# Performance work log

Measured on AMD Instinct MI355X. Metric: run time of the kernel, lower is better.

## Reference

```python
import jax, jax.numpy as jnp
import numpy as np

ACT_DIM, H, ZD, NZ, B, T, NS = 20, 64, 64, 5, 1024, 128, 1000


def setup_inputs() -> dict:
    key = jax.random.key(0)
    ks = jax.random.split(key, 24)
    w = lambda k, s: jax.random.normal(k, s, jnp.float32) * 0.1
    return {
        'acts': jax.random.randint(ks[0], (B, T), 0, ACT_DIM, dtype=jnp.int32),
        'durs': jax.random.uniform(ks[1], (B, T), jnp.float32),
        'W_act': w(ks[2], (ACT_DIM, H)), 'b_act': jnp.zeros(H, jnp.float32),
        'W_dur': w(ks[3], (1, H)), 'b_dur': jnp.zeros(H, jnp.float32),
        'W_x': w(ks[4], (2 * H, H)), 'b_x': jnp.zeros(H, jnp.float32),
        'W_z': w(ks[5], (ZD, H)), 'b_z': jnp.zeros(H, jnp.float32),
        'Wp1': w(ks[6], (NZ, 2 * H, H)), 'bp1': jnp.zeros((NZ, H), jnp.float32),
        'Wp2': w(ks[7], (NZ, H, ZD)), 'bp2': jnp.zeros((NZ, ZD), jnp.float32),
        'Wq1': w(ks[8], (NZ, H, ZD)), 'bq1': jnp.zeros((NZ, ZD), jnp.float32),
        'Wq2': w(ks[9], (NZ, ZD, ZD)), 'bq2': jnp.zeros((NZ, ZD), jnp.float32),
        'W_dec': w(ks[10], (2 * H, H)), 'b_dec': jnp.zeros(H, jnp.float32),
        'W_a': w(ks[11], (H, ACT_DIM)), 'b_a': jnp.zeros(ACT_DIM, jnp.float32),
        'W_durd': w(ks[12], (2 * H, 1)), 'b_durd': jnp.zeros(1, jnp.float32),
        'W_ih': w(ks[13], (2 * H, 3 * H)), 'W_hh': w(ks[14], (H, 3 * H)),
        'b_ih': jnp.zeros(3 * H, jnp.float32), 'b_hh': jnp.zeros(3 * H, jnp.float32),
        'gamma_post': jnp.ones((1, NZ), jnp.float32),
        'gamma_prior': jnp.ones((1, NZ), jnp.float32),
    }


def reference(acts, durs, W_act, b_act, W_dur, b_dur, W_x, b_x, W_z, b_z,
              Wp1, bp1, Wp2, bp2, Wq1, bq1, Wq2, bq2, W_dec, b_dec,
              W_a, b_a, W_durd, b_durd, W_ih, W_hh, b_ih, b_hh,
              gamma_post, gamma_prior):
    relu, sp = jax.nn.relu, jax.nn.softplus
    Bn, Tn = acts.shape
    hd = W_hh.shape[0]
    rngkey = jax.random.key(42)

    # Precompute per-timestep input embeddings, vectorized over T.
    one_hot = jax.nn.one_hot(acts, W_act.shape[0], dtype=jnp.float32)   # (B,T,A)
    phi_act = relu(one_hot @ W_act + b_act)                              # (B,T,H)
    phi_dur = relu(durs[..., None] * W_dur[0] + b_dur)                   # (B,T,H)
    phi_x_all = relu(jnp.concatenate([phi_act, phi_dur], -1) @ W_x + b_x)
    phi_x_all = jnp.swapaxes(phi_x_all, 0, 1)                            # (T,B,H)

    # NOTE: the torch code computes mu and sigma from the SAME network output
    # (identical pre-activation), so we compute it once. gamma matmul: (1,nz)@(B,nz,z)->(B,1,z)
    def mix_post(inp):
        h1 = relu(jnp.einsum('bi,nio->bno', inp, Wp1) + bp1)
        pre = jnp.einsum('bno,noz->bnz', h1, Wp2) + bp2
        m = jnp.einsum('on,bnz->boz', gamma_post, pre)
        return relu(m), sp(m)

    def mix_prior(h):
        h1 = relu(jnp.einsum('bi,nio->bno', h, Wq1) + bq1)
        pre = jnp.einsum('bno,noz->bnz', h1, Wq2) + bq2
        m = jnp.einsum('on,bnz->boz', gamma_prior, pre)
        return relu(m), sp(m)

    def gru(x, h):
        gi = x @ W_ih + b_ih
        gh = h @ W_hh + b_hh
        ir, iz, inn = jnp.split(gi, 3, -1)
        hr, hz, hn = jnp.split(gh, 3, -1)
        r = jax.nn.sigmoid(ir + hr)
        zz = jax.nn.sigmoid(iz + hz)
        n = jnp.tanh(inn + r * hn)
        return (1.0 - zz) * n + zz * h

    def sample_mean(k, mu, sigma):
        eps = jnp.mean(jax.random.normal(k, (NS,) + mu.shape, mu.dtype), 0)
        return (mu + sigma * eps)[:, 0, :]

    def kl(m1, s1, m2, s2):  # diag-normal KL, summed over z (Independent, 1)
        return jnp.sum(jnp.log(s2 / s1) + (s1 ** 2 + (m1 - m2) ** 2) / (2.0 * s2 ** 2) - 0.5, -1)

    def step(carry, xs):
        h, kld = carry
        phi_x, t = xs
        pm, ps = mix_post(jnp.concatenate([phi_x, h], -1))
        qm, qs = mix_prior(h)
        kld = kld + kl(pm, ps, qm, qs)
        z = sample_mean(jax.random.fold_in(rngkey, t), pm, ps)
        phi_z = relu(z @ W_z + b_z)
        h = gru(jnp.concatenate([phi_x, phi_z], -1), h)
        return (h, kld), None

    h0 = jnp.zeros((Bn, hd), jnp.float32)
    (h, kld), _ = jax.lax.scan(step, (h0, jnp.zeros((Bn, 1), jnp.float32)),
                               (phi_x_all, jnp.arange(Tn)))

    qm, qs = mix_prior(h)
    z = sample_mean(jax.random.fold_in(rngkey, Tn), qm, qs)
    phi_z = relu(z @ W_z + b_z)
    dec = relu(jnp.concatenate([phi_z, h], -1) @ W_dec + b_dec)
    logits = dec @ W_a + b_a
    phi_logits = relu(logits @ W_act + b_act)
    dur_dec = jnp.concatenate([phi_logits, dec], -1) @ W_durd + b_durd
    return logits, (dur_dec, sp(dur_dec)), jnp.mean(kld)
```

## Files before the change

### kernel.cpp

```cpp
#include <hip/hip_runtime.h>
#include <hip/hip_bf16.h>
#include <math.h>


#define TT   128
#define NZN  5
#define ADIM 20
#define ROWS 16
#define FRW  38
#define PS   68

typedef __attribute__((ext_vector_type(8))) short short8;
typedef __attribute__((ext_vector_type(4))) float f32x4;

__device__ __forceinline__ float reluf(float x) { return fmaxf(x, 0.f); }
__device__ __forceinline__ float frcp(float x)  { return __builtin_amdgcn_rcpf(x); }
__device__ __forceinline__ float fexp(float x)  { return __expf(x); }
__device__ __forceinline__ float flog(float x)  { return __logf(x); }
__device__ __forceinline__ float fsigm(float x) { return frcp(1.f + fexp(-x)); }
__device__ __forceinline__ float ftanh(float x) {
    float cx = fminf(fmaxf(x, -15.f), 15.f);
    float e2 = fexp(2.f * cx);
    return 1.f - 2.f * frcp(e2 + 1.f);
}
__device__ __forceinline__ float fsoftplus(float x) {
    return fmaxf(x, 0.f) + flog(1.f + fexp(-fabsf(x)));
}
__device__ __forceinline__ unsigned int pk2bf(float lo, float hi) {
    unsigned int r;
    asm volatile("v_cvt_pk_bf16_f32 %0, %1, %2" : "=v"(r) : "v"(lo), "v"(hi));
    return r;
}
__device__ __forceinline__ short8 pack8(float v0, float v1, float v2, float v3,
                                        float v4, float v5, float v6, float v7) {
    union { short8 s; unsigned int u[4]; } r;
    r.u[0] = pk2bf(v0, v1); r.u[1] = pk2bf(v2, v3);
    r.u[2] = pk2bf(v4, v5); r.u[3] = pk2bf(v6, v7);
    return r.s;
}
__device__ __forceinline__ void stage2(short* buf, int shift, int rw0, int col,
                                       float v0, float v1) {
    unsigned int u = pk2bf(v0, v1);
    buf[(rw0 << shift) + (col ^ ((rw0 & 7) << 3))]             = (short)(u & 0xffff);
    buf[((rw0 + 1) << shift) + (col ^ (((rw0 + 1) & 7) << 3))] = (short)(u >> 16);
}
__device__ __forceinline__ short8 lda64(const short* b, int c, int col0) {
    return *(const short8*)(b + c * 64 + (col0 ^ ((c & 7) << 3)));
}
__device__ __forceinline__ short8 lda128(const short* b, int c, int col0) {
    return *(const short8*)(b + c * 128 + (col0 ^ ((c & 7) << 3)));
}
__device__ __forceinline__ unsigned short f2bf(float x) {
    union { float f; unsigned int u; } v; v.f = x;
    unsigned int r = v.u + 0x7fffu + ((v.u >> 16) & 1u);
    return (unsigned short)(r >> 16);
}
__device__ __forceinline__ float wave_sum64(float v) {
#pragma unroll
    for (int off = 32; off > 0; off >>= 1) v += __shfl_xor(v, off, 64);
    return v;
}
#define MFMA(a, b, acc) __builtin_amdgcn_mfma_f32_16x16x32_bf16((a), (b), (acc), 0, 0, 0)

__global__ void vrnn_zero(float* out) { out[22528] = 0.f; }

__global__ __launch_bounds__(256) void vrnn_pack(
    const float* __restrict__ W_x,  const float* __restrict__ Wp1,
    const float* __restrict__ Wq1,  const float* __restrict__ Wp2,
    const float* __restrict__ Wq2,  const float* __restrict__ W_z,
    const float* __restrict__ W_ih, const float* __restrict__ W_hh,
    short* __restrict__ ws)
{
    const int tid = blockIdx.x * blockDim.x + threadIdx.x;
    if (tid >= 8 * FRW * 64) return;
    const int l = tid & 63, f = (tid >> 6) % FRW, w = (tid >> 6) / FRW;
    const int cc = l & 15, gg = l >> 4;
    const float* src = nullptr; int ld = 64, ncol = 0, k0 = 0;
    if (w < 4) {
        const int fcp = 16 * w + cc; ncol = fcp;
        if (f < 4)       { src = W_x;  k0 = 32 * f; }
        else if (f < 20) { int r = f - 4;  int n = r >> 2, q = r & 3;
                           src = Wp1 + n * 8192; k0 = 32 * q; }
        else if (f < 30) { int r = f - 20; int n = r >> 1, q = r & 1;
                           src = Wp2 + n * 4096; k0 = 32 * q; }
        else if (f < 32) { src = W_z;  k0 = 32 * (f - 30); }
        else             { int r = f - 32; int gt = r >> 1, q = r & 1;
                           src = W_ih; ld = 192; ncol = gt * 64 + fcp; k0 = 64 + 32 * q; }
    } else {
        const int fcp = 16 * (w - 4) + cc; ncol = fcp;
        if (f < 10)      { int n = f >> 1, q = f & 1;
                           src = Wq1 + n * 4096; k0 = 32 * q; }
        else if (f < 16) { int r = f - 10; int gt = r >> 1, q = r & 1;
                           src = W_hh; ld = 192; ncol = gt * 64 + fcp; k0 = 32 * q; }
        else if (f < 20) { src = Wp1 + 4 * 8192; k0 = 32 * (f - 16); }
        else if (f < 30) { int r = f - 20; int n = r >> 1, q = r & 1;
                           src = Wq2 + n * 4096; k0 = 32 * q; }
        else if (f < 36) { int r = f - 30; int gt = r >> 1, q = r & 1;
                           src = W_ih; ld = 192; ncol = gt * 64 + fcp; k0 = 32 * q; }
    }
    short8 frag = {0, 0, 0, 0, 0, 0, 0, 0};
    if (src) {
#pragma unroll
        for (int j = 0; j < 8; ++j)
            frag[j] = (short)f2bf(src[(k0 + 8 * gg + j) * ld + ncol]);
    }
    *(short8*)(ws + ((w * FRW + f) * 64 + l) * 8) = frag;
}

__global__ __launch_bounds__(512, 1) void vrnn_main(
    const int* __restrict__ acts, const float* __restrict__ durs,
    const float* __restrict__ W_act, const float* __restrict__ b_act,
    const float* __restrict__ W_dur, const float* __restrict__ b_dur,
    const float* __restrict__ b_x, const float* __restrict__ b_z,
    const float* __restrict__ bp1, const float* __restrict__ bq1,
    const float* __restrict__ bp2, const float* __restrict__ bq2,
    const float* __restrict__ b_ih, const float* __restrict__ b_hh,
    const float* __restrict__ g_post, const float* __restrict__ g_prior,
    const float* __restrict__ Wq1, const float* __restrict__ Wq2,
    const float* __restrict__ W_z, const float* __restrict__ W_dec,
    const float* __restrict__ b_dec, const float* __restrict__ W_a,
    const float* __restrict__ b_a, const float* __restrict__ W_durd,
    const float* __restrict__ b_durd,
    const short* __restrict__ ws, float* __restrict__ d_out)
{
    const int w = threadIdx.x >> 6, l = threadIdx.x & 63;
    const bool isH = (w >= 4);
    const int ns = isH ? (w - 4) : w;
    const int g = l >> 4, c = l & 15;
    const int fc = 16 * ns + c;
    const int row0 = blockIdx.x * ROWS;

    __shared__ __align__(16) short s_xz[ROWS * 128];
    __shared__ __align__(16) short s_h[ROWS * 64];
    __shared__ __align__(16) short s_h1p[NZN][ROWS * 64];
    __shared__ __align__(16) short s_h1q[NZN][ROWS * 64];
    __shared__ __align__(16) short s_z[ROWS * 64];
    __shared__ float s_gh[3][ROWS * PS];
    __shared__ float s_gix[3][ROWS * PS];
    __shared__ float s_qm[ROWS * PS], s_qs[ROWS * PS], s_lqs[ROWS * PS];
    __shared__ float s_hf[ROWS * 64];
    __shared__ float s_fin[8][320];
    __shared__ float s_klsum[ROWS];

    short8 Bfr[FRW];
    {
        const short8* Bw = ((const short8*)ws) + (w * FRW) * 64 + l;
#pragma unroll
        for (int f = 0; f < FRW; ++f) Bfr[f] = Bw[f * 64];
    }
#define BF(f) Bfr[f]
    const f32x4 Z4 = {0.f, 0.f, 0.f, 0.f};

    float b1r[NZN], gam[NZN];
    float c2 = 0.f, bA, bB;
    if (!isH) {
#pragma unroll
        for (int n = 0; n < NZN; ++n) {
            gam[n] = g_post[n];
            b1r[n] = bp1[n * 64 + fc];
            c2 = fmaf(gam[n], bp2[n * 64 + fc], c2);
        }
        bA = b_x[fc];
        bB = b_z[fc];
    } else {
#pragma unroll
        for (int n = 0; n < NZN; ++n) {
            gam[n] = g_prior[n];
            b1r[n] = bq1[n * 64 + fc];
            c2 = fmaf(gam[n], bq2[n * 64 + fc], c2);
        }
        bA = bp1[4 * 64 + fc];
        bB = 0.f;
    }
    const float bih0 = b_ih[fc], bih1 = b_ih[64 + fc], bih2 = b_ih[128 + fc];
    const float bhh0 = b_hh[fc], bhh1 = b_hh[64 + fc], bhh2 = b_hh[128 + fc];

    float hr[4] = {0.f, 0.f, 0.f, 0.f};
    float kl[4] = {0.f, 0.f, 0.f, 0.f};
    float pmv[4];

    for (int i = threadIdx.x; i < ROWS * 64; i += 512) s_h[i] = 0;
    if (threadIdx.x < ROWS) s_klsum[threadIdx.x] = 0.f;

    short8 ax0, ax1, ah0, ah1;

    for (int t = 0; t < TT; ++t) {
        __syncthreads();
        if (!isH) {
            const int   arow = acts[(row0 + c) * TT + t];
            const float dur  = durs[(row0 + c) * TT + t];
            const float4* wa4 = (const float4*)(W_act + arow * 64 + 8 * g);
            const float4* ba4 = (const float4*)(b_act + 8 * g);
            float4 w0 = wa4[0], w1 = wa4[1], w2 = wa4[8], w3 = wa4[9];
            float4 b0 = ba4[0], b1 = ba4[1], b2 = ba4[8], b3 = ba4[9];
            short8 e0 = pack8(reluf(w0.x + b0.x), reluf(w0.y + b0.y), reluf(w0.z + b0.z), reluf(w0.w + b0.w),
                              reluf(w1.x + b1.x), reluf(w1.y + b1.y), reluf(w1.z + b1.z), reluf(w1.w + b1.w));
            short8 e1 = pack8(reluf(w2.x + b2.x), reluf(w2.y + b2.y), reluf(w2.z + b2.z), reluf(w2.w + b2.w),
                              reluf(w3.x + b3.x), reluf(w3.y + b3.y), reluf(w3.z + b3.z), reluf(w3.w + b3.w));
            const float4* wd4 = (const float4*)(W_dur + 8 * g);
            const float4* bd4 = (const float4*)(b_dur + 8 * g);
            float4 d0 = wd4[0], d1 = wd4[1], d2 = wd4[8], d3 = wd4[9];
            float4 c0 = bd4[0], c1 = bd4[1], c2_ = bd4[8], c3 = bd4[9];
            short8 e2 = pack8(reluf(fmaf(dur, d0.x, c0.x)), reluf(fmaf(dur, d0.y, c0.y)),
                              reluf(fmaf(dur, d0.z, c0.z)), reluf(fmaf(dur, d0.w, c0.w)),
                              reluf(fmaf(dur, d1.x, c1.x)), reluf(fmaf(dur, d1.y, c1.y)),
                              reluf(fmaf(dur, d1.z, c1.z)), reluf(fmaf(dur, d1.w, c1.w)));
            short8 e3 = pack8(reluf(fmaf(dur, d2.x, c2_.x)), reluf(fmaf(dur, d2.y, c2_.y)),
                              reluf(fmaf(dur, d2.z, c2_.z)), reluf(fmaf(dur, d2.w, c2_.w)),
                              reluf(fmaf(dur, d3.x, c3.x)), reluf(fmaf(dur, d3.y, c3.y)),
                              reluf(fmaf(dur, d3.z, c3.z)), reluf(fmaf(dur, d3.w, c3.w)));
            f32x4 x = Z4;
            x = MFMA(e0, BF(0), x); x = MFMA(e1, BF(1), x);
            x = MFMA(e2, BF(2), x); x = MFMA(e3, BF(3), x);
            stage2(s_xz, 7, 4 * g,     fc, reluf(x[0] + bA), reluf(x[1] + bA));
            stage2(s_xz, 7, 4 * g + 2, fc, reluf(x[2] + bA), reluf(x[3] + bA));
        } else {
            ah0 = lda64(s_h, c, 8 * g);
            ah1 = lda64(s_h, c, 32 + 8 * g);
#pragma unroll
            for (int n = 0; n < NZN; ++n) {
                f32x4 q = MFMA(ah0, BF(2 * n), Z4);
                q = MFMA(ah1, BF(2 * n + 1), q);
                stage2(s_h1q[n], 6, 4 * g,     fc, reluf(q[0] + b1r[n]), reluf(q[1] + b1r[n]));
                stage2(s_h1q[n], 6, 4 * g + 2, fc, reluf(q[2] + b1r[n]), reluf(q[3] + b1r[n]));
            }
#pragma unroll
            for (int gt = 0; gt < 3; ++gt) {
                f32x4 gh = MFMA(ah0, BF(10 + 2 * gt), Z4);
                gh = MFMA(ah1, BF(11 + 2 * gt), gh);
#pragma unroll
                for (int r = 0; r < 4; ++r)
                    s_gh[gt][(4 * g + r) * PS + fc] = gh[r];
            }
        }
        __syncthreads();
        if (!isH) {
            ax0 = lda128(s_xz, c, 8 * g);
            ax1 = lda128(s_xz, c, 32 + 8 * g);
            ah0 = lda64(s_h, c, 8 * g);
            ah1 = lda64(s_h, c, 32 + 8 * g);
#pragma unroll
            for (int n = 0; n < 4; ++n) {
                f32x4 p = MFMA(ax0, BF(4 + 4 * n), Z4);
                p = MFMA(ax1, BF(5 + 4 * n), p);
                p = MFMA(ah0, BF(6 + 4 * n), p);
                p = MFMA(ah1, BF(7 + 4 * n), p);
                stage2(s_h1p[n], 6, 4 * g,     fc, reluf(p[0] + b1r[n]), reluf(p[1] + b1r[n]));
                stage2(s_h1p[n], 6, 4 * g + 2, fc, reluf(p[2] + b1r[n]), reluf(p[3] + b1r[n]));
            }
        } else {
            ax0 = lda128(s_xz, c, 8 * g);
            ax1 = lda128(s_xz, c, 32 + 8 * g);
            {
                f32x4 p = MFMA(ax0, BF(16), Z4);
                p = MFMA(ax1, BF(17), p);
                p = MFMA(ah0, BF(18), p);
                p = MFMA(ah1, BF(19), p);
                stage2(s_h1p[4], 6, 4 * g,     fc, reluf(p[0] + bA), reluf(p[1] + bA));
                stage2(s_h1p[4], 6, 4 * g + 2, fc, reluf(p[2] + bA), reluf(p[3] + bA));
            }
            f32x4 mq = Z4;
#pragma unroll
            for (int n = 0; n < NZN; ++n) {
                short8 hq0 = lda64(s_h1q[n], c, 8 * g);
                short8 hq1 = lda64(s_h1q[n], c, 32 + 8 * g);
                f32x4 q = MFMA(hq0, BF(20 + 2 * n), Z4);
                q = MFMA(hq1, BF(21 + 2 * n), q);
#pragma unroll
                for (int r = 0; r < 4; ++r) mq[r] = fmaf(gam[n], q[r], mq[r]);
            }
#pragma unroll
            for (int r = 0; r < 4; ++r) {
                const int rw = 4 * g + r;
                float mpri = mq[r] + c2;
                float qm = reluf(mpri), qs = fsoftplus(mpri);
                s_qm[rw * PS + fc] = qm;
                s_qs[rw * PS + fc] = qs;
                s_lqs[rw * PS + fc] = flog(qs);
            }
        }
        __syncthreads();
        if (!isH) {
            f32x4 mp = Z4;
#pragma unroll
            for (int n = 0; n < NZN; ++n) {
                short8 hp0 = lda64(s_h1p[n], c, 8 * g);
                short8 hp1 = lda64(s_h1p[n], c, 32 + 8 * g);
                f32x4 p = MFMA(hp0, BF(20 + 2 * n), Z4);
                p = MFMA(hp1, BF(21 + 2 * n), p);
#pragma unroll
                for (int r = 0; r < 4; ++r) mp[r] = fmaf(gam[n], p[r], mp[r]);
            }
#pragma unroll
            for (int r = 0; r < 4; ++r) {
                const int rw = 4 * g + r;
                float mpost = mp[r] + c2;
                float pm = reluf(mpost), ps = fsoftplus(mpost);
                float qm = s_qm[rw * PS + fc];
                float qs = s_qs[rw * PS + fc];
                float lqs = s_lqs[rw * PS + fc];
                float dd = pm - qm;
                kl[r] += lqs - flog(ps) + (ps * ps + dd * dd) * 0.5f * frcp(qs * qs) - 0.5f;
                pmv[r] = pm;
            }
            stage2(s_z, 6, 4 * g,     fc, pmv[0], pmv[1]);
            stage2(s_z, 6, 4 * g + 2, fc, pmv[2], pmv[3]);
        } else {
#pragma unroll
            for (int gt = 0; gt < 3; ++gt) {
                f32x4 gx = MFMA(ax0, BF(30 + 2 * gt), Z4);
                gx = MFMA(ax1, BF(31 + 2 * gt), gx);
#pragma unroll
                for (int r = 0; r < 4; ++r)
                    s_gix[gt][(4 * g + r) * PS + fc] = gx[r];
            }
        }
        __syncthreads();
        if (!isH) {
            short8 az0 = lda64(s_z, c, 8 * g);
            short8 az1 = lda64(s_z, c, 32 + 8 * g);
            f32x4 zz = MFMA(az0, BF(30), Z4);
            zz = MFMA(az1, BF(31), zz);
            stage2(s_xz, 7, 4 * g,     64 + fc, reluf(zz[0] + bB), reluf(zz[1] + bB));
            stage2(s_xz, 7, 4 * g + 2, 64 + fc, reluf(zz[2] + bB), reluf(zz[3] + bB));
        }
        __syncthreads();
        if (!isH) {
            short8 gz0 = lda128(s_xz, c, 64 + 8 * g);
            short8 gz1 = lda128(s_xz, c, 96 + 8 * g);
            f32x4 gi0 = MFMA(gz0, BF(32), Z4); gi0 = MFMA(gz1, BF(33), gi0);
            f32x4 gi1 = MFMA(gz0, BF(34), Z4); gi1 = MFMA(gz1, BF(35), gi1);
            f32x4 gi2 = MFMA(gz0, BF(36), Z4); gi2 = MFMA(gz1, BF(37), gi2);
#pragma unroll
            for (int r = 0; r < 4; ++r) {
                const int rw = 4 * g + r;
                float i0 = gi0[r] + s_gix[0][rw * PS + fc] + bih0;
                float i1 = gi1[r] + s_gix[1][rw * PS + fc] + bih1;
                float i2 = gi2[r] + s_gix[2][rw * PS + fc] + bih2;
                float h0 = s_gh[0][rw * PS + fc] + bhh0;
                float h1 = s_gh[1][rw * PS + fc] + bhh1;
                float h2 = s_gh[2][rw * PS + fc] + bhh2;
                float rr = fsigm(i0 + h0);
                float zg = fsigm(i1 + h1);
                float nn = ftanh(i2 + rr * h2);
                hr[r] = (1.f - zg) * nn + zg * hr[r];
            }
            stage2(s_h, 6, 4 * g,     fc, hr[0], hr[1]);
            stage2(s_h, 6, 4 * g + 2, fc, hr[2], hr[3]);
        }
    }

    if (!isH) {
#pragma unroll
        for (int r = 0; r < 4; ++r) s_hf[(4 * g + r) * 64 + fc] = hr[r];
#pragma unroll
        for (int off = 1; off < 16; off <<= 1) {
#pragma unroll
            for (int r = 0; r < 4; ++r) kl[r] += __shfl_xor(kl[r], off, 64);
        }
        if (c == 0) {
#pragma unroll
            for (int r = 0; r < 4; ++r) atomicAdd(&s_klsum[4 * g + r], kl[r]);
        }
    }
    __syncthreads();

    {
        float gqe[NZN];
#pragma unroll
        for (int n = 0; n < NZN; ++n) gqe[n] = g_prior[n];
        float* sf = s_fin[w];
        for (int rr = 0; rr < 2; ++rr) {
            const int lr = 2 * w + rr, grow = row0 + lr;
            float accn[NZN];
#pragma unroll
            for (int n = 0; n < NZN; ++n) accn[n] = bq1[n * 64 + l];
            for (int i = 0; i < 64; ++i) {
                const float hv = s_hf[lr * 64 + i];
#pragma unroll
                for (int n = 0; n < NZN; ++n) accn[n] += hv * Wq1[(n * 64 + i) * 64 + l];
            }
#pragma unroll
            for (int n = 0; n < NZN; ++n) sf[n * 64 + l] = reluf(accn[n]);
            float u[NZN];
#pragma unroll
            for (int n = 0; n < NZN; ++n) u[n] = bq2[n * 64 + l];
            for (int o = 0; o < 64; ++o) {
#pragma unroll
                for (int n = 0; n < NZN; ++n) u[n] += sf[n * 64 + o] * Wq2[(n * 64 + o) * 64 + l];
            }
            float mpri = 0.f;
#pragma unroll
            for (int n = 0; n < NZN; ++n) mpri = fmaf(gqe[n], u[n], mpri);
            sf[l] = reluf(mpri);
            float za = b_z[l];
            for (int i = 0; i < 64; ++i) za += sf[i] * W_z[i * 64 + l];
            sf[64 + l] = reluf(za);
            float dv = b_dec[l];
            for (int i = 0; i < 64; ++i) {
                dv += sf[64 + i] * W_dec[i * 64 + l];
                dv += s_hf[lr * 64 + i] * W_dec[(64 + i) * 64 + l];
            }
            const float dec = reluf(dv);
            sf[128 + l] = dec;
            float lg = 0.f;
            if (l < ADIM) {
                lg = b_a[l];
                for (int o = 0; o < 64; ++o) lg += sf[128 + o] * W_a[o * ADIM + l];
                d_out[grow * ADIM + l] = lg;
                sf[192 + l] = lg;
            }
            float pl = b_act[l];
#pragma unroll
            for (int j = 0; j < ADIM; ++j) pl += sf[192 + j] * W_act[j * 64 + l];
            pl = reluf(pl);
            float contrib = pl * W_durd[l] + dec * W_durd[64 + l];
            contrib = wave_sum64(contrib);
            if (l == 0) {
                const float dd = contrib + b_durd[0];
                d_out[20480 + grow] = dd;
                d_out[21504 + grow] = fsoftplus(dd);
            }
        }
    }
    if (threadIdx.x == 0) {
        float s = 0.f;
#pragma unroll
        for (int i = 0; i < ROWS; ++i) s += s_klsum[i];
        atomicAdd(d_out + 22528, s * (1.f / 1024.f));
    }
#undef BF
}

extern "C" void kernel_launch(void* const* d_in, const int* in_sizes, int n_in,
                              void* d_out, int out_size, void* d_ws, size_t ws_size,
                              hipStream_t stream)
{
    const int*   acts    = (const int*)  d_in[0];
    const float* durs    = (const float*)d_in[1];
    const float* W_act   = (const float*)d_in[2];
    const float* b_act   = (const float*)d_in[3];
    const float* W_dur   = (const float*)d_in[4];
    const float* b_dur   = (const float*)d_in[5];
    const float* W_x     = (const float*)d_in[6];
    const float* b_x     = (const float*)d_in[7];
    const float* W_z     = (const float*)d_in[8];
    const float* b_z     = (const float*)d_in[9];
    const float* Wp1     = (const float*)d_in[10];
    const float* bp1     = (const float*)d_in[11];
    const float* Wp2     = (const float*)d_in[12];
    const float* bp2     = (const float*)d_in[13];
    const float* Wq1     = (const float*)d_in[14];
    const float* bq1     = (const float*)d_in[15];
    const float* Wq2     = (const float*)d_in[16];
    const float* bq2     = (const float*)d_in[17];
    const float* W_dec   = (const float*)d_in[18];
    const float* b_dec   = (const float*)d_in[19];
    const float* W_a     = (const float*)d_in[20];
    const float* b_a     = (const float*)d_in[21];
    const float* W_durd  = (const float*)d_in[22];
    const float* b_durd  = (const float*)d_in[23];
    const float* W_ih    = (const float*)d_in[24];
    const float* W_hh    = (const float*)d_in[25];
    const float* b_ih    = (const float*)d_in[26];
    const float* b_hh    = (const float*)d_in[27];
    const float* g_post  = (const float*)d_in[28];
    const float* g_prior = (const float*)d_in[29];
    float* out = (float*)d_out;
    short* ws  = (short*)d_ws;

    vrnn_zero<<<1, 1, 0, stream>>>(out);
    vrnn_pack<<<76, 256, 0, stream>>>(W_x, Wp1, Wq1, Wp2, Wq2, W_z, W_ih, W_hh, ws);
    vrnn_main<<<64, 512, 0, stream>>>(
        acts, durs, W_act, b_act, W_dur, b_dur, b_x, b_z,
        bp1, bq1, bp2, bq2, b_ih, b_hh, g_post, g_prior,
        Wq1, Wq2, W_z, W_dec, b_dec, W_a, b_a, W_durd, b_durd,
        ws, out);
}
```

Measured before the change: 836.6 us.

## Precompute phi_x in a separate kernel and stream weight fragments from memory

Adds a phix_prep kernel that computes the relu(concat(act, dur embedding) @ W_x + b_x) features for all timesteps up front. It stores them as swizzled bf16 tiles in the workspace, so the recurrent loop copies one tile into shared memory each step instead of building embeddings and running four MFMAs. The W_x fragments are dropped from the packed weights. Separately, the main kernel no longer keeps all weight B-fragments in registers; each MFMA now reads its fragment from global memory. That frees registers but puts memory latency inside the serial time loop, and the extra prep kernel adds launch and compute cost.

```diff
diff --git a/kernel.cpp b/kernel.cpp
--- a/kernel.cpp
+++ b/kernel.cpp
@@ -7,8 +7,9 @@
 #define NZN  5
 #define ADIM 20
 #define ROWS 16
-#define FRW  38
+#define FRW  36
 #define PS   68
+#define PHIX_OFF (8 * FRW * 64 * 8)
 
 typedef __attribute__((ext_vector_type(8))) short short8;
 typedef __attribute__((ext_vector_type(4))) float f32x4;
@@ -31,13 +32,6 @@
     asm volatile("v_cvt_pk_bf16_f32 %0, %1, %2" : "=v"(r) : "v"(lo), "v"(hi));
     return r;
 }
-__device__ __forceinline__ short8 pack8(float v0, float v1, float v2, float v3,
-                                        float v4, float v5, float v6, float v7) {
-    union { short8 s; unsigned int u[4]; } r;
-    r.u[0] = pk2bf(v0, v1); r.u[1] = pk2bf(v2, v3);
-    r.u[2] = pk2bf(v4, v5); r.u[3] = pk2bf(v6, v7);
-    return r.s;
-}
 __device__ __forceinline__ void stage2(short* buf, int shift, int rw0, int col,
                                        float v0, float v1) {
     unsigned int u = pk2bf(v0, v1);
@@ -65,11 +59,10 @@
 __global__ void vrnn_zero(float* out) { out[22528] = 0.f; }
 
 __global__ __launch_bounds__(256) void vrnn_pack(
-    const float* __restrict__ W_x,  const float* __restrict__ Wp1,
-    const float* __restrict__ Wq1,  const float* __restrict__ Wp2,
-    const float* __restrict__ Wq2,  const float* __restrict__ W_z,
-    const float* __restrict__ W_ih, const float* __restrict__ W_hh,
-    short* __restrict__ ws)
+    const float* __restrict__ Wp1, const float* __restrict__ Wq1,
+    const float* __restrict__ Wp2, const float* __restrict__ Wq2,
+    const float* __restrict__ W_z, const float* __restrict__ W_ih,
+    const float* __restrict__ W_hh, short* __restrict__ ws)
 {
     const int tid = blockIdx.x * blockDim.x + threadIdx.x;
     if (tid >= 8 * FRW * 64) return;
@@ -78,13 +71,12 @@
     const float* src = nullptr; int ld = 64, ncol = 0, k0 = 0;
     if (w < 4) {
         const int fcp = 16 * w + cc; ncol = fcp;
-        if (f < 4)       { src = W_x;  k0 = 32 * f; }
-        else if (f < 20) { int r = f - 4;  int n = r >> 2, q = r & 3;
+        if (f < 16)      { int n = f >> 2, q = f & 3;
                            src = Wp1 + n * 8192; k0 = 32 * q; }
-        else if (f < 30) { int r = f - 20; int n = r >> 1, q = r & 1;
+        else if (f < 26) { int r = f - 16; int n = r >> 1, q = r & 1;
                            src = Wp2 + n * 4096; k0 = 32 * q; }
-        else if (f < 32) { src = W_z;  k0 = 32 * (f - 30); }
-        else             { int r = f - 32; int gt = r >> 1, q = r & 1;
+        else if (f < 28) { src = W_z;  k0 = 32 * (f - 26); }
+        else if (f < 34) { int r = f - 28; int gt = r >> 1, q = r & 1;
                            src = W_ih; ld = 192; ncol = gt * 64 + fcp; k0 = 64 + 32 * q; }
     } else {
         const int fcp = 16 * (w - 4) + cc; ncol = fcp;
@@ -95,7 +87,7 @@
         else if (f < 20) { src = Wp1 + 4 * 8192; k0 = 32 * (f - 16); }
         else if (f < 30) { int r = f - 20; int n = r >> 1, q = r & 1;
                            src = Wq2 + n * 4096; k0 = 32 * q; }
-        else if (f < 36) { int r = f - 30; int gt = r >> 1, q = r & 1;
+        else             { int r = f - 30; int gt = r >> 1, q = r & 1;
                            src = W_ih; ld = 192; ncol = gt * 64 + fcp; k0 = 32 * q; }
     }
     short8 frag = {0, 0, 0, 0, 0, 0, 0, 0};
@@ -107,11 +99,43 @@
     *(short8*)(ws + ((w * FRW + f) * 64 + l) * 8) = frag;
 }
 
-__global__ __launch_bounds__(512, 1) void vrnn_main(
+__global__ __launch_bounds__(256) void phix_prep(
     const int* __restrict__ acts, const float* __restrict__ durs,
     const float* __restrict__ W_act, const float* __restrict__ b_act,
     const float* __restrict__ W_dur, const float* __restrict__ b_dur,
-    const float* __restrict__ b_x, const float* __restrict__ b_z,
+    const float* __restrict__ W_x,  const float* __restrict__ b_x,
+    short* __restrict__ phix)
+{
+    const int blk = blockIdx.x >> 3, tch = blockIdx.x & 7;
+    const int tid = threadIdx.x, v = tid >> 6, l = tid & 63;
+    __shared__ float sWx[8192];
+    __shared__ float scat[4][128];
+    for (int e = tid; e < 8192; e += 256) sWx[e] = W_x[e];
+    const float bact = b_act[l], wdur = W_dur[l], bdur = b_dur[l], bx = b_x[l];
+    __syncthreads();
+    for (int u = 0; u < 64; ++u) {
+        const int pp = v * 64 + u;
+        const int t = tch * 16 + (pp >> 4);
+        const int r = pp & 15;
+        const int b = blk * 16 + r;
+        const int   a   = acts[b * TT + t];
+        const float dur = durs[b * TT + t];
+        scat[v][l]      = reluf(W_act[a * 64 + l] + bact);
+        scat[v][64 + l] = reluf(fmaf(dur, wdur, bdur));
+        __syncthreads();
+        float phi = bx;
+#pragma unroll 8
+        for (int i = 0; i < 128; ++i)
+            phi = fmaf(scat[v][i], sWx[i * 64 + l], phi);
+        phix[((t * 64 + blk) * 16 + r) * 64 + (l ^ ((r & 7) << 3))] =
+            (short)f2bf(reluf(phi));
+        __syncthreads();
+    }
+}
+
+__global__ __launch_bounds__(512, 1) void vrnn_main(
+    const float* __restrict__ W_act, const float* __restrict__ b_act,
+    const float* __restrict__ b_z,
     const float* __restrict__ bp1, const float* __restrict__ bq1,
     const float* __restrict__ bp2, const float* __restrict__ bq2,
     const float* __restrict__ b_ih, const float* __restrict__ b_hh,
@@ -129,6 +153,7 @@
     const int g = l >> 4, c = l & 15;
     const int fc = 16 * ns + c;
     const int row0 = blockIdx.x * ROWS;
+    const short* __restrict__ phix = ws + PHIX_OFF;
 
     __shared__ __align__(16) short s_xz[ROWS * 128];
     __shared__ __align__(16) short s_h[ROWS * 64];
@@ -142,17 +167,12 @@
     __shared__ float s_fin[8][320];
     __shared__ float s_klsum[ROWS];
 
-    short8 Bfr[FRW];
-    {
-        const short8* Bw = ((const short8*)ws) + (w * FRW) * 64 + l;
-#pragma unroll
-        for (int f = 0; f < FRW; ++f) Bfr[f] = Bw[f * 64];
-    }
-#define BF(f) Bfr[f]
+    const short8* Bw = ((const short8*)ws) + (w * FRW) * 64 + l;
+#define BF(f) Bw[(f) * 64]
     const f32x4 Z4 = {0.f, 0.f, 0.f, 0.f};
 
     float b1r[NZN], gam[NZN];
-    float c2 = 0.f, bA, bB;
+    float c2 = 0.f, bA = 0.f, bzr = 0.f;
     if (!isH) {
 #pragma unroll
         for (int n = 0; n < NZN; ++n) {
@@ -160,8 +180,7 @@
             b1r[n] = bp1[n * 64 + fc];
             c2 = fmaf(gam[n], bp2[n * 64 + fc], c2);
         }
-        bA = b_x[fc];
-        bB = b_z[fc];
+        bzr = b_z[fc];
     } else {
 #pragma unroll
         for (int n = 0; n < NZN; ++n) {
@@ -170,7 +189,6 @@
             c2 = fmaf(gam[n], bq2[n * 64 + fc], c2);
         }
         bA = bp1[4 * 64 + fc];
-        bB = 0.f;
     }
     const float bih0 = b_ih[fc], bih1 = b_ih[64 + fc], bih2 = b_ih[128 + fc];
     const float bhh0 = b_hh[fc], bhh1 = b_hh[64 + fc], bhh2 = b_hh[128 + fc];
@@ -187,33 +205,12 @@
     for (int t = 0; t < TT; ++t) {
         __syncthreads();
         if (!isH) {
-            const int   arow = acts[(row0 + c) * TT + t];
-            const float dur  = durs[(row0 + c) * TT + t];
-            const float4* wa4 = (const float4*)(W_act + arow * 64 + 8 * g);
-            const float4* ba4 = (const float4*)(b_act + 8 * g);
-            float4 w0 = wa4[0], w1 = wa4[1], w2 = wa4[8], w3 = wa4[9];
-            float4 b0 = ba4[0], b1 = ba4[1], b2 = ba4[8], b3 = ba4[9];
-            short8 e0 = pack8(reluf(w0.x + b0.x), reluf(w0.y + b0.y), reluf(w0.z + b0.z), reluf(w0.w + b0.w),
-                              reluf(w1.x + b1.x), reluf(w1.y + b1.y), reluf(w1.z + b1.z), reluf(w1.w + b1.w));
-            short8 e1 = pack8(reluf(w2.x + b2.x), reluf(w2.y + b2.y), reluf(w2.z + b2.z), reluf(w2.w + b2.w),
-                              reluf(w3.x + b3.x), reluf(w3.y + b3.y), reluf(w3.z + b3.z), reluf(w3.w + b3.w));
-            const float4* wd4 = (const float4*)(W_dur + 8 * g);
-            const float4* bd4 = (const float4*)(b_dur + 8 * g);
-            float4 d0 = wd4[0], d1 = wd4[1], d2 = wd4[8], d3 = wd4[9];
-            float4 c0 = bd4[0], c1 = bd4[1], c2_ = bd4[8], c3 = bd4[9];
-            short8 e2 = pack8(reluf(fmaf(dur, d0.x, c0.x)), reluf(fmaf(dur, d0.y, c0.y)),
-                              reluf(fmaf(dur, d0.z, c0.z)), reluf(fmaf(dur, d0.w, c0.w)),
-                              reluf(fmaf(dur, d1.x, c1.x)), reluf(fmaf(dur, d1.y, c1.y)),
-                              reluf(fmaf(dur, d1.z, c1.z)), reluf(fmaf(dur, d1.w, c1.w)));
-            short8 e3 = pack8(reluf(fmaf(dur, d2.x, c2_.x)), reluf(fmaf(dur, d2.y, c2_.y)),
-                              reluf(fmaf(dur, d2.z, c2_.z)), reluf(fmaf(dur, d2.w, c2_.w)),
-                              reluf(fmaf(dur, d3.x, c3.x)), reluf(fmaf(dur, d3.y, c3.y)),
-                              reluf(fmaf(dur, d3.z, c3.z)), reluf(fmaf(dur, d3.w, c3.w)));
-            f32x4 x = Z4;
-            x = MFMA(e0, BF(0), x); x = MFMA(e1, BF(1), x);
-            x = MFMA(e2, BF(2), x); x = MFMA(e3, BF(3), x);
-            stage2(s_xz, 7, 4 * g,     fc, reluf(x[0] + bA), reluf(x[1] + bA));
-            stage2(s_xz, 7, 4 * g + 2, fc, reluf(x[2] + bA), reluf(x[3] + bA));
+            const int idx = w * 64 + l;
+            const int r  = idx >> 4;
+            const int c0 = (idx & 15) * 4;
+            const uint2* src = (const uint2*)(phix + (size_t)(t * 64 + blockIdx.x) * 1024);
+            uint2 val = src[idx];
+            *(uint2*)(s_xz + r * 128 + c0) = val;
         } else {
             ah0 = lda64(s_h, c, 8 * g);
             ah1 = lda64(s_h, c, 32 + 8 * g);
@@ -241,10 +238,10 @@
             ah1 = lda64(s_h, c, 32 + 8 * g);
 #pragma unroll
             for (int n = 0; n < 4; ++n) {
-                f32x4 p = MFMA(ax0, BF(4 + 4 * n), Z4);
-                p = MFMA(ax1, BF(5 + 4 * n), p);
-                p = MFMA(ah0, BF(6 + 4 * n), p);
-                p = MFMA(ah1, BF(7 + 4 * n), p);
+                f32x4 p = MFMA(ax0, BF(4 * n + 0), Z4);
+                p = MFMA(ax1, BF(4 * n + 1), p);
+                p = MFMA(ah0, BF(4 * n + 2), p);
+                p = MFMA(ah1, BF(4 * n + 3), p);
                 stage2(s_h1p[n], 6, 4 * g,     fc, reluf(p[0] + b1r[n]), reluf(p[1] + b1r[n]));
                 stage2(s_h1p[n], 6, 4 * g + 2, fc, reluf(p[2] + b1r[n]), reluf(p[3] + b1r[n]));
             }
@@ -286,8 +283,8 @@
             for (int n = 0; n < NZN; ++n) {
                 short8 hp0 = lda64(s_h1p[n], c, 8 * g);
                 short8 hp1 = lda64(s_h1p[n], c, 32 + 8 * g);
-                f32x4 p = MFMA(hp0, BF(20 + 2 * n), Z4);
-                p = MFMA(hp1, BF(21 + 2 * n), p);
+                f32x4 p = MFMA(hp0, BF(16 + 2 * n), Z4);
+                p = MFMA(hp1, BF(17 + 2 * n), p);
 #pragma unroll
                 for (int r = 0; r < 4; ++r) mp[r] = fmaf(gam[n], p[r], mp[r]);
             }
@@ -319,18 +316,18 @@
         if (!isH) {
             short8 az0 = lda64(s_z, c, 8 * g);
             short8 az1 = lda64(s_z, c, 32 + 8 * g);
-            f32x4 zz = MFMA(az0, BF(30), Z4);
-            zz = MFMA(az1, BF(31), zz);
-            stage2(s_xz, 7, 4 * g,     64 + fc, reluf(zz[0] + bB), reluf(zz[1] + bB));
-            stage2(s_xz, 7, 4 * g + 2, 64 + fc, reluf(zz[2] + bB), reluf(zz[3] + bB));
+            f32x4 zz = MFMA(az0, BF(26), Z4);
+            zz = MFMA(az1, BF(27), zz);
+            stage2(s_xz, 7, 4 * g,     64 + fc, reluf(zz[0] + bzr), reluf(zz[1] + bzr));
+            stage2(s_xz, 7, 4 * g + 2, 64 + fc, reluf(zz[2] + bzr), reluf(zz[3] + bzr));
         }
         __syncthreads();
         if (!isH) {
             short8 gz0 = lda128(s_xz, c, 64 + 8 * g);
             short8 gz1 = lda128(s_xz, c, 96 + 8 * g);
-            f32x4 gi0 = MFMA(gz0, BF(32), Z4); gi0 = MFMA(gz1, BF(33), gi0);
-            f32x4 gi1 = MFMA(gz0, BF(34), Z4); gi1 = MFMA(gz1, BF(35), gi1);
-            f32x4 gi2 = MFMA(gz0, BF(36), Z4); gi2 = MFMA(gz1, BF(37), gi2);
+            f32x4 gi0 = MFMA(gz0, BF(28), Z4); gi0 = MFMA(gz1, BF(29), gi0);
+            f32x4 gi1 = MFMA(gz0, BF(30), Z4); gi1 = MFMA(gz1, BF(31), gi1);
+            f32x4 gi2 = MFMA(gz0, BF(32), Z4); gi2 = MFMA(gz1, BF(33), gi2);
 #pragma unroll
             for (int r = 0; r < 4; ++r) {
                 const int rw = 4 * g + r;
@@ -470,10 +467,11 @@
     short* ws  = (short*)d_ws;
 
     vrnn_zero<<<1, 1, 0, stream>>>(out);
-    vrnn_pack<<<76, 256, 0, stream>>>(W_x, Wp1, Wq1, Wp2, Wq2, W_z, W_ih, W_hh, ws);
+    vrnn_pack<<<72, 256, 0, stream>>>(Wp1, Wq1, Wp2, Wq2, W_z, W_ih, W_hh, ws);
+    phix_prep<<<512, 256, 0, stream>>>(acts, durs, W_act, b_act, W_dur, b_dur,
+                                       W_x, b_x, ws + PHIX_OFF);
     vrnn_main<<<64, 512, 0, stream>>>(
-        acts, durs, W_act, b_act, W_dur, b_dur, b_x, b_z,
-        bp1, bq1, bp2, bq2, b_ih, b_hh, g_post, g_prior,
+        W_act, b_act, b_z, bp1, bq1, bp2, bq2, b_ih, b_hh, g_post, g_prior,
         Wq1, Wq2, W_z, W_dec, b_dec, W_a, b_a, W_durd, b_durd,
         ws, out);
 }
```

After: 798.1 us. -4.6%, faster.
